# Optimization experiments

Measured on AMD Instinct MI355X. Metric: run time of the kernel, lower is better.

## Reference

```python
import jax, jax.numpy as jnp
import numpy as np

TOP_K = 2


def setup_inputs() -> dict:
    key = jax.random.key(0)
    k1, k2, k3, k4 = jax.random.split(key, 4)
    B, S, H, I, E = 8, 2048, 768, 3072, 8
    x = jax.random.normal(k1, (B, S, H), dtype=jnp.float32)
    # kaiming_uniform-ish scale for weights
    router_w = jax.random.uniform(k2, (E, H), dtype=jnp.float32, minval=-1.0, maxval=1.0) * (1.0 / np.sqrt(H))
    up_w = jax.random.uniform(k3, (E, H, I), dtype=jnp.float32, minval=-1.0, maxval=1.0) * (1.0 / np.sqrt(H))
    down_w = jax.random.uniform(k4, (E, I, H), dtype=jnp.float32, minval=-1.0, maxval=1.0) * (1.0 / np.sqrt(I))
    return {"x": x, "router_w": router_w, "up_w": up_w, "down_w": down_w}


def reference(x, router_w, up_w, down_w):
    B, S, H = x.shape
    E = up_w.shape[0]
    T = B * S
    xf = x.reshape(T, H)
    # router: Linear(H -> E, bias=False) then softmax, top-k, renormalize
    logits = xf @ router_w.T                      # [T, E]
    probs = jax.nn.softmax(logits, axis=-1)
    top_w, top_i = jax.lax.top_k(probs, TOP_K)    # [T, K]
    top_w = top_w / jnp.sum(top_w, axis=-1, keepdims=True)
    # dense per-(token, expert) gate: zero for unselected experts
    gate = jnp.zeros((T, E), dtype=xf.dtype).at[jnp.arange(T)[:, None], top_i].add(top_w)
    # combine: sum_e gate[:, e] * down_e(gelu(up_e(x)))
    out = jnp.zeros_like(xf)
    for e in range(E):  # fixed small expert count; loop is structural, not over data dims
        h = jax.nn.gelu(xf @ up_w[e], approximate=False)   # exact GELU == torch F.gelu
        out = out + gate[:, e:e + 1] * (h @ down_w[e])
    return out.reshape(B, S, H)
```

## Files before the change

### kernel.cpp

```cpp
#include <hip/hip_runtime.h>

typedef short bf16x8 __attribute__((ext_vector_type(8)));
typedef float f32x4  __attribute__((ext_vector_type(4)));

#define T_TOK 16384
#define HD 768
#define ID 3072
#define NE 8

__device__ __forceinline__ unsigned short f2bf(float f) {
    unsigned int u = __float_as_uint(f);
    unsigned int r = (u + 0x7FFFu + ((u >> 16) & 1u)) >> 16;
    return (unsigned short)r;
}

__device__ __forceinline__ void gload16(const void* g, void* l) {
    __builtin_amdgcn_global_load_lds(
        (const __attribute__((address_space(1))) void*)g,
        (__attribute__((address_space(3))) void*)l, 16, 0, 0);
}

__global__ __launch_bounds__(256) void k_cvt_x(const float* __restrict__ x,
                                               unsigned short* __restrict__ xb) {
    int i = blockIdx.x * 256 + threadIdx.x;
    float4 v = ((const float4*)x)[i];
    ushort4 o;
    o.x = f2bf(v.x); o.y = f2bf(v.y); o.z = f2bf(v.z); o.w = f2bf(v.w);
    ((ushort4*)xb)[i] = o;
}

__global__ __launch_bounds__(256) void k_tp(const float* __restrict__ in,
                                            unsigned short* __restrict__ out,
                                            int R, int C) {
    __shared__ float t[64][65];
    const float* ine = in + (size_t)blockIdx.z * R * C;
    unsigned short* oute = out + (size_t)blockIdx.z * R * C;
    int c0 = blockIdx.x * 64, r0 = blockIdx.y * 64;
    int lc = threadIdx.x & 63, lr4 = threadIdx.x >> 6;
#pragma unroll
    for (int i = 0; i < 16; i++) {
        int r = i * 4 + lr4;
        t[r][lc] = ine[(size_t)(r0 + r) * C + c0 + lc];
    }
    __syncthreads();
#pragma unroll
    for (int i = 0; i < 16; i++) {
        int r = i * 4 + lr4;
        oute[(size_t)(c0 + r) * R + r0 + lc] = f2bf(t[lc][r]);
    }
}

__global__ __launch_bounds__(256) void k_router(const float* __restrict__ x,
                                                const float* __restrict__ rw,
                                                int* __restrict__ topE,
                                                float* __restrict__ topW) {
    __shared__ float lrw[NE * HD];
    for (int i = threadIdx.x; i < NE * HD; i += 256) lrw[i] = rw[i];
    __syncthreads();
    int lane = threadIdx.x & 63;
    int t = blockIdx.x * 4 + (threadIdx.x >> 6);
    const float* xr = x + (size_t)t * HD;
    float acc[NE] = {0, 0, 0, 0, 0, 0, 0, 0};
    for (int h = lane; h < HD; h += 64) {
        float xv = xr[h];
#pragma unroll
        for (int e = 0; e < NE; e++) acc[e] = fmaf(xv, lrw[e * HD + h], acc[e]);
    }
#pragma unroll
    for (int e = 0; e < NE; e++) {
        float v = acc[e];
#pragma unroll
        for (int o = 32; o > 0; o >>= 1) v += __shfl_xor(v, o, 64);
        acc[e] = v;
    }
    if (lane == 0) {
        int e1 = 0; float l1 = acc[0];
#pragma unroll
        for (int e = 1; e < NE; e++) if (acc[e] > l1) { l1 = acc[e]; e1 = e; }
        int e2 = -1; float l2 = -1e30f;
#pragma unroll
        for (int e = 0; e < NE; e++) if (e != e1 && acc[e] > l2) { l2 = acc[e]; e2 = e; }
        float ex = expf(l2 - l1);
        float w1 = 1.0f / (1.0f + ex);
        topE[2 * t] = e1; topE[2 * t + 1] = e2;
        topW[2 * t] = w1; topW[2 * t + 1] = ex * w1;
    }
}

__global__ __launch_bounds__(256) void k_scatter(const int* __restrict__ topE,
                                                 const float* __restrict__ topW,
                                                 int* __restrict__ counts,
                                                 int* __restrict__ tokL,
                                                 float* __restrict__ gateL) {
    __shared__ int lc[NE], lbase[NE];
    if (threadIdx.x < NE) lc[threadIdx.x] = 0;
    __syncthreads();
    int t = blockIdx.x * 256 + threadIdx.x;
    int e1 = topE[2 * t], e2 = topE[2 * t + 1];
    int p1 = atomicAdd(&lc[e1], 1);
    int p2 = atomicAdd(&lc[e2], 1);
    __syncthreads();
    if (threadIdx.x < NE) lbase[threadIdx.x] = atomicAdd(&counts[threadIdx.x], lc[threadIdx.x]);
    __syncthreads();
    int q1 = lbase[e1] + p1, q2 = lbase[e2] + p2;
    tokL[e1 * T_TOK + q1] = t;  gateL[e1 * T_TOK + q1] = topW[2 * t];
    tokL[e2 * T_TOK + q2] = t;  gateL[e2 * T_TOK + q2] = topW[2 * t + 1];
}

__global__ __launch_bounds__(512, 2) void k_moe(
    const unsigned short* __restrict__ xb,
    const unsigned short* __restrict__ upt,
    const unsigned short* __restrict__ dnt,
    const int* __restrict__ counts,
    const int* __restrict__ tokL,
    const float* __restrict__ gateL,
    float* __restrict__ out) {
    __shared__ __align__(16) char lds[155648];
    char* xs = lds;
    char* hs = lds + 98304;
    char* ring = lds + 106496;

    const int e = blockIdx.x & 7;
    const int slot = blockIdx.x >> 3;
    const int cnt = counts[e];
    if (slot * 64 >= cnt) return;
    const int nrow = min(64, cnt - slot * 64);
    const int* tok = tokL + e * T_TOK + slot * 64;
    const float* gat = gateL + e * T_TOK + slot * 64;

    const int tid = threadIdx.x;
    const int lane = tid & 63;
    const int wid = tid >> 6;
    const int mi = wid >> 2, ni = wid & 3;

    const char* upe = (const char*)(upt + (size_t)e * ID * HD);
    const char* dne = (const char*)(dnt + (size_t)e * HD * ID);

    {
        int off = tid * 16;
#pragma unroll
        for (int s = 0; s < 12; s++) {
            int o = off + s * 8192;
            int m = o / 1536;
            int cb = o - m * 1536;
            int tk = (m < nrow) ? tok[m] : tok[0];
            const char* src = (const char*)xb + (size_t)tk * 1536 + (size_t)(cb ^ ((m & 7) << 4));
            gload16(src, xs + s * 8192 + wid * 1024);
        }
    }
    asm volatile("s_waitcnt vmcnt(0)" ::: "memory");
    __builtin_amdgcn_s_barrier();
    asm volatile("" ::: "memory");

    auto issue = [&](int s) {
        char* dst = ring + (s % 6) * 8192 + wid * 1024;
        int ci = s / 24;
        int ph = s - ci * 24;
        int row = tid >> 3;
        int cb = (tid & 7) << 4;
        int scb = cb ^ ((row & 7) << 4);
        const char* src;
        if (ci >= 48) src = upe;
        else if (ph < 12) src = upe + (size_t)(ci * 64 + row) * 1536 + ph * 128 + scb;
        else              src = dne + (size_t)((ph - 12) * 64 + row) * 6144 + ci * 128 + scb;
        gload16(src, dst);
    };

    f32x4 acc[2][12];
#pragma unroll
    for (int a = 0; a < 2; a++)
#pragma unroll
        for (int b = 0; b < 12; b++) acc[a][b] = (f32x4){0.f, 0.f, 0.f, 0.f};

    issue(0); issue(1); issue(2); issue(3);

    f32x4 acch[2];
    bf16x8 ha[2][2];

    for (int ci = 0; ci < 48; ci++) {
#pragma unroll
        for (int ks = 0; ks < 12; ks++) {
            issue(ci * 24 + ks + 4);
            asm volatile("s_waitcnt vmcnt(4)" ::: "memory");
            __builtin_amdgcn_s_barrier();
            asm volatile("" ::: "memory");
            char* buf = ring + (ks % 6) * 8192;
            if (ks == 0) { acch[0] = (f32x4){0.f,0.f,0.f,0.f}; acch[1] = (f32x4){0.f,0.f,0.f,0.f}; }
#pragma unroll
            for (int kr = 0; kr < 2; kr++) {
                int bn = ni * 16 + (lane & 15);
                int bo = ((kr * 32 + (lane >> 4) * 8) * 2) ^ ((bn & 7) << 4);
                bf16x8 bfrag = *(const bf16x8*)(buf + bn * 128 + bo);
#pragma unroll
                for (int mr = 0; mr < 2; mr++) {
                    int ar = mi * 32 + mr * 16 + (lane & 15);
                    int ao = ((ks * 64 + kr * 32 + (lane >> 4) * 8) * 2) ^ ((ar & 7) << 4);
                    bf16x8 afrag = *(const bf16x8*)(xs + ar * 1536 + ao);
                    acch[mr] = __builtin_amdgcn_mfma_f32_16x16x32_bf16(afrag, bfrag, acch[mr], 0, 0, 0);
                }
            }
            if (ks == 11) {
#pragma unroll
                for (int mr = 0; mr < 2; mr++) {
                    int col = ni * 16 + (lane & 15);
#pragma unroll
                    for (int r = 0; r < 4; r++) {
                        int m = mi * 32 + mr * 16 + (lane >> 4) * 4 + r;
                        float v = acch[mr][r];
                        float g = 0.5f * v * (1.0f + erff(v * 0.70710678118f));
                        *(unsigned short*)(hs + m * 128 + ((col * 2) ^ ((m & 7) << 4))) = f2bf(g);
                    }
                }
                asm volatile("s_waitcnt lgkmcnt(0)" ::: "memory");
            }
        }
#pragma unroll
        for (int j = 0; j < 12; j++) {
            issue(ci * 24 + 12 + j + 4);
            asm volatile("s_waitcnt vmcnt(4)" ::: "memory");
            __builtin_amdgcn_s_barrier();
            asm volatile("" ::: "memory");
            char* buf = ring + ((12 + j) % 6) * 8192;
            if (j == 0) {
#pragma unroll
                for (int mr = 0; mr < 2; mr++)
#pragma unroll
                    for (int kr = 0; kr < 2; kr++) {
                        int ar = mi * 32 + mr * 16 + (lane & 15);
                        int ao = ((kr * 32 + (lane >> 4) * 8) * 2) ^ ((ar & 7) << 4);
                        ha[mr][kr] = *(const bf16x8*)(hs + ar * 128 + ao);
                    }
            }
#pragma unroll
            for (int kr = 0; kr < 2; kr++) {
                int bn = ni * 16 + (lane & 15);
                int bo = ((kr * 32 + (lane >> 4) * 8) * 2) ^ ((bn & 7) << 4);
                bf16x8 bfrag = *(const bf16x8*)(buf + bn * 128 + bo);
#pragma unroll
                for (int mr = 0; mr < 2; mr++)
                    acc[mr][j] = __builtin_amdgcn_mfma_f32_16x16x32_bf16(ha[mr][kr], bfrag, acc[mr][j], 0, 0, 0);
            }
        }
    }

    int   t4[2][4];
    float g4[2][4];
#pragma unroll
    for (int mr = 0; mr < 2; mr++)
#pragma unroll
        for (int r = 0; r < 4; r++) {
            int m = mi * 32 + mr * 16 + (lane >> 4) * 4 + r;
            bool valid = m < nrow;
            t4[mr][r] = valid ? tok[m] : -1;
            g4[mr][r] = valid ? gat[m] : 0.f;
        }
#pragma unroll
    for (int mr = 0; mr < 2; mr++)
#pragma unroll
        for (int j = 0; j < 12; j++) {
            int colg = j * 64 + ni * 16 + (lane & 15);
#pragma unroll
            for (int r = 0; r < 4; r++) {
                if (t4[mr][r] >= 0)
                    atomicAdd(out + (size_t)t4[mr][r] * HD + colg, g4[mr][r] * acc[mr][j][r]);
            }
        }
}

extern "C" void kernel_launch(void* const* d_in, const int* in_sizes, int n_in,
                              void* d_out, int out_size, void* d_ws, size_t ws_size,
                              hipStream_t stream) {
    const float* x  = (const float*)d_in[0];
    const float* rw = (const float*)d_in[1];
    const float* uw = (const float*)d_in[2];
    const float* dw = (const float*)d_in[3];
    float* out = (float*)d_out;

    char* w = (char*)d_ws;
    unsigned short* xb  = (unsigned short*)w; w += (size_t)T_TOK * HD * 2;
    unsigned short* upt = (unsigned short*)w; w += (size_t)NE * ID * HD * 2;
    unsigned short* dnt = (unsigned short*)w; w += (size_t)NE * HD * ID * 2;
    int*   topE   = (int*)w;   w += (size_t)T_TOK * 2 * 4;
    float* topW   = (float*)w; w += (size_t)T_TOK * 2 * 4;
    int*   counts = (int*)w;   w += 256;
    int*   tokL   = (int*)w;   w += (size_t)NE * T_TOK * 4;
    float* gateL  = (float*)w; w += (size_t)NE * T_TOK * 4;

    hipMemsetAsync(d_out, 0, (size_t)T_TOK * HD * 4, stream);
    hipMemsetAsync(counts, 0, 256, stream);

    k_cvt_x<<<(T_TOK * HD) / (256 * 4), 256, 0, stream>>>(x, xb);
    k_tp<<<dim3(ID / 64, HD / 64, NE), 256, 0, stream>>>(uw, upt, HD, ID);
    k_tp<<<dim3(HD / 64, ID / 64, NE), 256, 0, stream>>>(dw, dnt, ID, HD);
    k_router<<<T_TOK / 4, 256, 0, stream>>>(x, rw, topE, topW);
    k_scatter<<<T_TOK / 256, 256, 0, stream>>>(topE, topW, counts, tokL, gateL);
    k_moe<<<2048, 512, 0, stream>>>(xb, upt, dnt, counts, tokL, gateL, out);
}
```

Measured before the change: 779.4 us.

## Split fused MoE into two grouped GEMMs with materialized bf16 intermediate

Replaces the fused per-64-token up+GELU+down kernel with a tile-descriptor pass and two separate grouped GEMM kernels that use 256x256 tiles. The GELU output is written to a global bf16 buffer and read back by the second GEMM. Larger tiles raise weight reuse and MFMA density, at the cost of extra global traffic for the intermediate. The exact erff is also swapped for a polynomial erf approximation. The new path runs only when the workspace is large enough; otherwise the fused kernel is kept.

```diff
diff --git a/kernel.cpp b/kernel.cpp
--- a/kernel.cpp
+++ b/kernel.cpp
@@ -7,6 +7,7 @@
 #define HD 768
 #define ID 3072
 #define NE 8
+#define NT1MAX 136
 
 __device__ __forceinline__ unsigned short f2bf(float f) {
     unsigned int u = __float_as_uint(f);
@@ -18,6 +19,16 @@
     __builtin_amdgcn_global_load_lds(
         (const __attribute__((address_space(1))) void*)g,
         (__attribute__((address_space(3))) void*)l, 16, 0, 0);
+}
+
+__device__ __forceinline__ float gelu_f(float x) {
+    float z = fabsf(x) * 0.70710678118f;
+    float t = 1.0f / fmaf(0.3275911f, z, 1.0f);
+    float p = t * fmaf(t, fmaf(t, fmaf(t, fmaf(t, 1.061405429f, -1.453152027f),
+                                       1.421413741f), -0.284496736f), 0.254829592f);
+    float e = 1.0f - p * __expf(-z * z);
+    float erfv = (x >= 0.f) ? e : -e;
+    return 0.5f * x * (1.0f + erfv);
 }
 
 __global__ __launch_bounds__(256) void k_cvt_x(const float* __restrict__ x,
@@ -107,6 +118,233 @@
     tokL[e2 * T_TOK + q2] = t;  gateL[e2 * T_TOK + q2] = topW[2 * t + 1];
 }
 
+__global__ void k_desc(const int* __restrict__ counts, int* __restrict__ tileE,
+                       int* __restrict__ tileM0, int* __restrict__ tileHB) {
+    if (threadIdx.x == 0 && blockIdx.x == 0) {
+        int off = 0, tl = 0;
+        for (int e = 0; e < NE; e++) {
+            int c = counts[e];
+            int nt = (c + 255) >> 8;
+            for (int t = 0; t < nt; t++) {
+                tileE[tl] = e; tileM0[tl] = t << 8; tileHB[tl] = off + (t << 8); tl++;
+            }
+            off += c;
+        }
+        for (; tl < NT1MAX; tl++) { tileE[tl] = -1; tileM0[tl] = 0; tileHB[tl] = 0; }
+    }
+}
+
+__global__ __launch_bounds__(512, 2) void k_gemm1(
+    const unsigned short* __restrict__ xb,
+    const unsigned short* __restrict__ upt,
+    const int* __restrict__ tokL,
+    const int* __restrict__ counts,
+    const int* __restrict__ tileE,
+    const int* __restrict__ tileM0,
+    const int* __restrict__ tileHB,
+    unsigned short* __restrict__ h) {
+    __shared__ __align__(16) char lds[4][32768];
+    constexpr int NK = HD / 32;
+    constexpr int NWG = NT1MAX * 12;
+    int bid = blockIdx.x;
+    int L = (bid & 7) * (NWG >> 3) + (bid >> 3);
+    int mt = L / 12, nt = L - mt * 12;
+    int e = tileE[mt];
+    if (e < 0) return;
+    int m0 = tileM0[mt];
+    int hb = tileHB[mt];
+    int nrow = min(256, counts[e] - m0);
+    const int* tok = tokL + e * T_TOK + m0;
+    int n0 = nt * 256;
+
+    const int tid = threadIdx.x, lane = tid & 63, wid = tid >> 6;
+    const int wm = wid >> 2, wn = wid & 3;
+    const int g = lane >> 4, r = lane & 15;
+
+    int ar0 = wid * 16 + r;
+    int ar1 = 128 + wid * 16 + r;
+    const char* a0 = (const char*)(xb + (size_t)tok[ar0 < nrow ? ar0 : 0] * HD);
+    const char* a1 = (const char*)(xb + (size_t)tok[ar1 < nrow ? ar1 : 0] * HD);
+    const char* bsl = (const char*)(upt + (size_t)e * ID * HD);
+    const char* b0 = bsl + (size_t)(n0 + wid * 16 + r) * (HD * 2);
+    const char* b1 = bsl + (size_t)(n0 + 128 + wid * 16 + r) * (HD * 2);
+    const int dstoff = wid * 1024 + lane * 16;
+    const int koff = g * 16;
+
+    auto issue = [&](int step, int slot) {
+        char* base = &lds[slot][0];
+        int kb = step * 64 + koff;
+        gload16(a0 + kb, base + dstoff);
+        gload16(a1 + kb, base + 8192 + dstoff);
+        gload16(b0 + kb, base + 16384 + dstoff);
+        gload16(b1 + kb, base + 24576 + dstoff);
+    };
+
+    f32x4 acc[8][4];
+#pragma unroll
+    for (int m = 0; m < 8; m++)
+#pragma unroll
+        for (int n = 0; n < 4; n++) acc[m][n] = (f32x4){0.f, 0.f, 0.f, 0.f};
+
+    issue(0, 0); issue(1, 1); issue(2, 2);
+    asm volatile("s_waitcnt vmcnt(8)" ::: "memory");
+    __builtin_amdgcn_s_barrier();
+    asm volatile("" ::: "memory");
+
+    const int aoff = wm * 8192 + g * 256 + r * 16;
+    const int boff = 16384 + wn * 4096 + g * 256 + r * 16;
+
+    for (int k = 0; k < NK; k++) {
+        char* base = &lds[k & 3][0];
+        bf16x8 a[4], b[4];
+#pragma unroll
+        for (int n = 0; n < 4; n++) b[n] = *(const bf16x8*)(base + boff + n * 1024);
+#pragma unroll
+        for (int m = 0; m < 4; m++) a[m] = *(const bf16x8*)(base + aoff + m * 1024);
+        issue(min(k + 3, NK - 1), (k + 3) & 3);
+        __builtin_amdgcn_s_setprio(1);
+#pragma unroll
+        for (int m = 0; m < 4; m++)
+#pragma unroll
+            for (int n = 0; n < 4; n++)
+                acc[m][n] = __builtin_amdgcn_mfma_f32_16x16x32_bf16(a[m], b[n], acc[m][n], 0, 0, 0);
+        __builtin_amdgcn_s_setprio(0);
+#pragma unroll
+        for (int m = 0; m < 4; m++) a[m] = *(const bf16x8*)(base + aoff + (4 + m) * 1024);
+        __builtin_amdgcn_s_setprio(1);
+#pragma unroll
+        for (int m = 0; m < 4; m++)
+#pragma unroll
+            for (int n = 0; n < 4; n++)
+                acc[4 + m][n] = __builtin_amdgcn_mfma_f32_16x16x32_bf16(a[m], b[n], acc[4 + m][n], 0, 0, 0);
+        __builtin_amdgcn_s_setprio(0);
+        asm volatile("s_waitcnt vmcnt(8)" ::: "memory");
+        __builtin_amdgcn_s_barrier();
+        asm volatile("" ::: "memory");
+    }
+    asm volatile("s_waitcnt vmcnt(0)" ::: "memory");
+
+#pragma unroll
+    for (int m = 0; m < 8; m++)
+#pragma unroll
+        for (int j = 0; j < 4; j++) {
+            int rl = wm * 128 + m * 16 + g * 4 + j;
+            if (rl < nrow) {
+                unsigned short* hr = h + (size_t)(hb + rl) * ID + n0 + wn * 64 + r;
+#pragma unroll
+                for (int n = 0; n < 4; n++) hr[n * 16] = f2bf(gelu_f(acc[m][n][j]));
+            }
+        }
+}
+
+__global__ __launch_bounds__(512, 2) void k_gemm2(
+    const unsigned short* __restrict__ h,
+    const unsigned short* __restrict__ dnt,
+    const int* __restrict__ tokL,
+    const float* __restrict__ gateL,
+    const int* __restrict__ counts,
+    const int* __restrict__ tileE,
+    const int* __restrict__ tileM0,
+    const int* __restrict__ tileHB,
+    float* __restrict__ out) {
+    __shared__ __align__(16) char lds[4][32768];
+    constexpr int NK = ID / 32;
+    constexpr int NWG = NT1MAX * 3;
+    int bid = blockIdx.x;
+    int L = (bid & 7) * (NWG >> 3) + (bid >> 3);
+    int mt = L / 3, nt = L - mt * 3;
+    int e = tileE[mt];
+    if (e < 0) return;
+    int m0 = tileM0[mt];
+    int hb = tileHB[mt];
+    int nrow = min(256, counts[e] - m0);
+    const int* tok = tokL + e * T_TOK + m0;
+    const float* gat = gateL + e * T_TOK + m0;
+    int n0 = nt * 256;
+
+    const int tid = threadIdx.x, lane = tid & 63, wid = tid >> 6;
+    const int wm = wid >> 2, wn = wid & 3;
+    const int g = lane >> 4, r = lane & 15;
+
+    int ar0 = wid * 16 + r;
+    int ar1 = 128 + wid * 16 + r;
+    const char* a0 = (const char*)(h + (size_t)(hb + ar0) * ID);
+    const char* a1 = (const char*)(h + (size_t)(hb + ar1) * ID);
+    const char* bsl = (const char*)(dnt + (size_t)e * ID * HD);
+    const char* b0 = bsl + (size_t)(n0 + wid * 16 + r) * (ID * 2);
+    const char* b1 = bsl + (size_t)(n0 + 128 + wid * 16 + r) * (ID * 2);
+    const int dstoff = wid * 1024 + lane * 16;
+    const int koff = g * 16;
+
+    auto issue = [&](int step, int slot) {
+        char* base = &lds[slot][0];
+        int kb = step * 64 + koff;
+        gload16(a0 + kb, base + dstoff);
+        gload16(a1 + kb, base + 8192 + dstoff);
+        gload16(b0 + kb, base + 16384 + dstoff);
+        gload16(b1 + kb, base + 24576 + dstoff);
+    };
+
+    f32x4 acc[8][4];
+#pragma unroll
+    for (int m = 0; m < 8; m++)
+#pragma unroll
+        for (int n = 0; n < 4; n++) acc[m][n] = (f32x4){0.f, 0.f, 0.f, 0.f};
+
+    issue(0, 0); issue(1, 1); issue(2, 2);
+    asm volatile("s_waitcnt vmcnt(8)" ::: "memory");
+    __builtin_amdgcn_s_barrier();
+    asm volatile("" ::: "memory");
+
+    const int aoff = wm * 8192 + g * 256 + r * 16;
+    const int boff = 16384 + wn * 4096 + g * 256 + r * 16;
+
+    for (int k = 0; k < NK; k++) {
+        char* base = &lds[k & 3][0];
+        bf16x8 a[4], b[4];
+#pragma unroll
+        for (int n = 0; n < 4; n++) b[n] = *(const bf16x8*)(base + boff + n * 1024);
+#pragma unroll
+        for (int m = 0; m < 4; m++) a[m] = *(const bf16x8*)(base + aoff + m * 1024);
+        issue(min(k + 3, NK - 1), (k + 3) & 3);
+        __builtin_amdgcn_s_setprio(1);
+#pragma unroll
+        for (int m = 0; m < 4; m++)
+#pragma unroll
+            for (int n = 0; n < 4; n++)
+                acc[m][n] = __builtin_amdgcn_mfma_f32_16x16x32_bf16(a[m], b[n], acc[m][n], 0, 0, 0);
+        __builtin_amdgcn_s_setprio(0);
+#pragma unroll
+        for (int m = 0; m < 4; m++) a[m] = *(const bf16x8*)(base + aoff + (4 + m) * 1024);
+        __builtin_amdgcn_s_setprio(1);
+#pragma unroll
+        for (int m = 0; m < 4; m++)
+#pragma unroll
+            for (int n = 0; n < 4; n++)
+                acc[4 + m][n] = __builtin_amdgcn_mfma_f32_16x16x32_bf16(a[m], b[n], acc[4 + m][n], 0, 0, 0);
+        __builtin_amdgcn_s_setprio(0);
+        asm volatile("s_waitcnt vmcnt(8)" ::: "memory");
+        __builtin_amdgcn_s_barrier();
+        asm volatile("" ::: "memory");
+    }
+    asm volatile("s_waitcnt vmcnt(0)" ::: "memory");
+
+#pragma unroll
+    for (int m = 0; m < 8; m++)
+#pragma unroll
+        for (int j = 0; j < 4; j++) {
+            int rl = wm * 128 + m * 16 + g * 4 + j;
+            if (rl < nrow) {
+                int t = tok[rl];
+                float gv = gat[rl];
+                float* orow = out + (size_t)t * HD + n0 + wn * 64 + r;
+#pragma unroll
+                for (int n = 0; n < 4; n++)
+                    atomicAdd(orow + n * 16, gv * acc[m][n][j]);
+            }
+        }
+}
+
 __global__ __launch_bounds__(512, 2) void k_moe(
     const unsigned short* __restrict__ xb,
     const unsigned short* __restrict__ upt,
@@ -207,8 +445,7 @@
                     for (int r = 0; r < 4; r++) {
                         int m = mi * 32 + mr * 16 + (lane >> 4) * 4 + r;
                         float v = acch[mr][r];
-                        float g = 0.5f * v * (1.0f + erff(v * 0.70710678118f));
-                        *(unsigned short*)(hs + m * 128 + ((col * 2) ^ ((m & 7) << 4))) = f2bf(g);
+                        *(unsigned short*)(hs + m * 128 + ((col * 2) ^ ((m & 7) << 4))) = f2bf(gelu_f(v));
                     }
                 }
                 asm volatile("s_waitcnt lgkmcnt(0)" ::: "memory");
@@ -276,15 +513,26 @@
     const float* dw = (const float*)d_in[3];
     float* out = (float*)d_out;
 
-    char* w = (char*)d_ws;
-    unsigned short* xb  = (unsigned short*)w; w += (size_t)T_TOK * HD * 2;
-    unsigned short* upt = (unsigned short*)w; w += (size_t)NE * ID * HD * 2;
-    unsigned short* dnt = (unsigned short*)w; w += (size_t)NE * HD * ID * 2;
-    int*   topE   = (int*)w;   w += (size_t)T_TOK * 2 * 4;
-    float* topW   = (float*)w; w += (size_t)T_TOK * 2 * 4;
-    int*   counts = (int*)w;   w += 256;
-    int*   tokL   = (int*)w;   w += (size_t)NE * T_TOK * 4;
-    float* gateL  = (float*)w; w += (size_t)NE * T_TOK * 4;
+    size_t off = 0;
+    char* base = (char*)d_ws;
+    auto alloc = [&](size_t bytes) -> char* {
+        char* p = base + off;
+        off += (bytes + 1023) & ~(size_t)1023;
+        return p;
+    };
+    unsigned short* xb   = (unsigned short*)alloc((size_t)T_TOK * HD * 2);
+    unsigned short* upt  = (unsigned short*)alloc((size_t)NE * ID * HD * 2);
+    unsigned short* dnt  = (unsigned short*)alloc((size_t)NE * HD * ID * 2);
+    int*   topE   = (int*)alloc((size_t)T_TOK * 2 * 4);
+    float* topW   = (float*)alloc((size_t)T_TOK * 2 * 4);
+    int*   counts = (int*)alloc(256);
+    int*   tileE  = (int*)alloc(NT1MAX * 4);
+    int*   tileM0 = (int*)alloc(NT1MAX * 4);
+    int*   tileHB = (int*)alloc(NT1MAX * 4);
+    int*   tokL   = (int*)alloc((size_t)NE * T_TOK * 4);
+    float* gateL  = (float*)alloc((size_t)NE * T_TOK * 4);
+    unsigned short* h = (unsigned short*)alloc((size_t)(T_TOK * 2 + 256) * ID * 2);
+    size_t need = off;
 
     hipMemsetAsync(d_out, 0, (size_t)T_TOK * HD * 4, stream);
     hipMemsetAsync(counts, 0, 256, stream);
@@ -294,5 +542,12 @@
     k_tp<<<dim3(HD / 64, ID / 64, NE), 256, 0, stream>>>(dw, dnt, ID, HD);
     k_router<<<T_TOK / 4, 256, 0, stream>>>(x, rw, topE, topW);
     k_scatter<<<T_TOK / 256, 256, 0, stream>>>(topE, topW, counts, tokL, gateL);
-    k_moe<<<2048, 512, 0, stream>>>(xb, upt, dnt, counts, tokL, gateL, out);
-}
+
+    if (ws_size >= need) {
+        k_desc<<<1, 64, 0, stream>>>(counts, tileE, tileM0, tileHB);
+        k_gemm1<<<NT1MAX * 12, 512, 0, stream>>>(xb, upt, tokL, counts, tileE, tileM0, tileHB, h);
+        k_gemm2<<<NT1MAX * 3, 512, 0, stream>>>(h, dnt, tokL, gateL, counts, tileE, tileM0, tileHB, out);
+    } else {
+        k_moe<<<2048, 512, 0, stream>>>(xb, upt, dnt, counts, tokL, gateL, out);
+    }
+}
```

Result: no change. 770.2 us (-1.2%).
